# Kernel tuning notes

Hardware: AMD Instinct MI355X
Metric: run time of the kernel (lower is better)

The kernel has to match this reference:

```python
import jax, jax.numpy as jnp
import numpy as np

B, N, C, D = 64, 1024, 128, 64

def setup_inputs() -> dict:
    key = jax.random.key(0)
    ks = jax.random.split(key, 7)
    # kaiming_normal_ on weights (fan_in = C), default zero-ish biases kept as Linear default uniform; use small uniform
    std = float(np.sqrt(2.0 / C))
    bb = float(1.0 / np.sqrt(C))
    return {
        "x": jax.random.normal(ks[0], (B, N, C), jnp.float32),
        "Wq": jax.random.normal(ks[1], (C, D), jnp.float32) * std,
        "bq": jax.random.uniform(ks[2], (D,), jnp.float32, -bb, bb),
        "Wk": jax.random.normal(ks[3], (C, D), jnp.float32) * std,
        "bk": jax.random.uniform(ks[4], (D,), jnp.float32, -bb, bb),
        "Wv": jax.random.normal(ks[5], (C, D), jnp.float32) * std,
        "bv": jax.random.uniform(ks[6], (D,), jnp.float32, -bb, bb),
    }

def reference(x, Wq, bq, Wk, bk, Wv, bv):
    q = jax.nn.relu(jnp.einsum('bnc,cd->bnd', x, Wq) + bq)  # [B,N,D]
    k = jax.nn.relu(jnp.einsum('bnc,cd->bnd', x, Wk) + bk)
    v = jax.nn.relu(jnp.einsum('bnc,cd->bnd', x, Wv) + bv)
    scores = jnp.einsum('bnd,bmd->bnm', q, k) / jnp.sqrt(jnp.asarray(D, q.dtype))
    attn = jax.nn.softmax(scores, axis=-1)
    out = jnp.einsum('bnm,bmd->bnd', attn, v)
    return out + q
```

## Files before the change

kernel.cpp:

```cpp
#include <hip/hip_runtime.h>
#include <hip/hip_bf16.h>


#define Bsz 64
#define Nsz 1024
#define Csz 128
#define Dsz 64

typedef __attribute__((ext_vector_type(8))) short short8;
typedef __attribute__((ext_vector_type(4))) float f32x4;

__device__ __forceinline__ unsigned short f2bf(float f) {
    union { float f; unsigned u; } v; v.f = f;
    unsigned r = v.u + 0x7FFF + ((v.u >> 16) & 1);
    return (unsigned short)(r >> 16);
}
__device__ __forceinline__ float bf2f(unsigned short h) {
    union { unsigned u; float f; } v; v.u = ((unsigned)h) << 16;
    return v.f;
}
__device__ __forceinline__ unsigned pack_bf16rn(float lo, float hi) {
    unsigned ulo = __float_as_uint(lo) + 0x8000u;
    unsigned uhi = __float_as_uint(hi) + 0x8000u;
    return __builtin_amdgcn_perm(uhi, ulo, 0x07060302u);
}
__device__ __forceinline__ void gl_lds16(const void* gsrc, void* ldst) {
    __builtin_amdgcn_global_load_lds(
        (const __attribute__((address_space(1))) unsigned int*)gsrc,
        (__attribute__((address_space(3))) unsigned int*)ldst, 16, 0, 0);
}

#define SCq (0.125f * 1.44269504f)
#define INV_SC (1.0f / (0.125f * 1.44269504f))

__global__ __launch_bounds__(256) void wprep_kernel(
    const float* __restrict__ Wq, const float* __restrict__ Wk,
    const float* __restrict__ Wv, unsigned short* __restrict__ wfrag)
{
    int t = blockIdx.x * 256 + threadIdx.x;
    int lane = t & 63, ksi = (t >> 6) & 3, dt = t >> 8;
    int l16 = lane & 15, quad = lane >> 4;
    int d = dt * 16 + l16;
    int c0 = ksi * 32 + quad * 8;
    short8 h8, l8, k8, v8;
    #pragma unroll
    for (int j = 0; j < 8; j++) {
        float w = Wq[(c0 + j) * Dsz + d];
        unsigned short h = f2bf(w);
        h8[j] = (short)h;
        l8[j] = (short)f2bf(w - bf2f(h));
        k8[j] = (short)f2bf(Wk[(c0 + j) * Dsz + d]);
        v8[j] = (short)f2bf(Wv[(c0 + j) * Dsz + d]);
    }
    int idx = (dt * 4 + ksi) * 64 + lane;
    ((short8*)wfrag)[0 * 1024 + idx] = h8;
    ((short8*)wfrag)[1 * 1024 + idx] = l8;
    ((short8*)wfrag)[2 * 1024 + idx] = k8;
    ((short8*)wfrag)[3 * 1024 + idx] = v8;
}

__global__ __launch_bounds__(256) void qkv_kernel(
    const float* __restrict__ x, const unsigned short* __restrict__ wfrag,
    const float* __restrict__ bq, const float* __restrict__ bk,
    const float* __restrict__ bv,
    unsigned short* __restrict__ qs, unsigned short* __restrict__ ksc,
    unsigned short* __restrict__ vt)
{
    __shared__ short xh[8192];
    __shared__ short xl[8192];
    const int t    = threadIdx.x;
    const int lane = t & 63;
    const int l16  = lane & 15, quad = lane >> 4;
    const int dt   = t >> 6;
    const long rowbase = (long)blockIdx.x * 128;
    const int d = dt * 16 + l16;

    short8 wqh[4], wql[4], wkf[4], wvf[4];
    #pragma unroll
    for (int ksi = 0; ksi < 4; ksi++) {
        int idx = (dt * 4 + ksi) * 64 + lane;
        wqh[ksi] = ((const short8*)wfrag)[0 * 1024 + idx];
        wql[ksi] = ((const short8*)wfrag)[1 * 1024 + idx];
        wkf[ksi] = ((const short8*)wfrag)[2 * 1024 + idx];
        wvf[ksi] = ((const short8*)wfrag)[3 * 1024 + idx];
    }
    const float bqd = bq[d], bkd = bk[d], bvd = bv[d];
    const long b = rowbase >> 10;

    for (int chunk = 0; chunk < 2; chunk++) {
        const long rowc = rowbase + chunk * 64;
        if (chunk) __syncthreads();

        {
            const int row = t & 63;
            const float* xrow = x + (rowc + row) * Csz;
            #pragma unroll
            for (int p = 0; p < 4; p++) {
                int cb = (t >> 6) + p * 4;
                float4 a = *(const float4*)(xrow + cb * 8);
                float4 bb = *(const float4*)(xrow + cb * 8 + 4);
                float f[8] = {a.x, a.y, a.z, a.w, bb.x, bb.y, bb.z, bb.w};
                short8 hi, lo;
                #pragma unroll
                for (int i = 0; i < 8; i++) {
                    unsigned short h = f2bf(f[i]);
                    hi[i] = (short)h;
                    lo[i] = (short)f2bf(f[i] - bf2f(h));
                }
                int unit = ((row >> 4) * 4 + (cb >> 2)) * 64 + ((row & 15) | ((cb & 3) << 4));
                *(short8*)&xh[unit * 8] = hi;
                *(short8*)&xl[unit * 8] = lo;
            }
        }
        __syncthreads();

        f32x4 aq[4], ak[4], av[4];
        #pragma unroll
        for (int i = 0; i < 4; i++) {
            aq[i] = (f32x4){0.f, 0.f, 0.f, 0.f};
            ak[i] = (f32x4){0.f, 0.f, 0.f, 0.f};
            av[i] = (f32x4){0.f, 0.f, 0.f, 0.f};
        }
        #pragma unroll
        for (int ksi = 0; ksi < 4; ksi++) {
            #pragma unroll
            for (int rt = 0; rt < 4; rt++) {
                short8 ah = *(const short8*)&xh[((rt * 4 + ksi) * 64 + lane) * 8];
                short8 al = *(const short8*)&xl[((rt * 4 + ksi) * 64 + lane) * 8];
                aq[rt] = __builtin_amdgcn_mfma_f32_16x16x32_bf16(ah, wqh[ksi], aq[rt], 0, 0, 0);
                aq[rt] = __builtin_amdgcn_mfma_f32_16x16x32_bf16(al, wqh[ksi], aq[rt], 0, 0, 0);
                aq[rt] = __builtin_amdgcn_mfma_f32_16x16x32_bf16(ah, wql[ksi], aq[rt], 0, 0, 0);
                ak[rt] = __builtin_amdgcn_mfma_f32_16x16x32_bf16(ah, wkf[ksi], ak[rt], 0, 0, 0);
                av[rt] = __builtin_amdgcn_mfma_f32_16x16x32_bf16(ah, wvf[ksi], av[rt], 0, 0, 0);
            }
        }

        float vv[16];
        #pragma unroll
        for (int rt = 0; rt < 4; rt++) {
            #pragma unroll
            for (int r = 0; r < 4; r++) {
                long n = rowc + rt * 16 + quad * 4 + r;
                float q = fmaxf(aq[rt][r] + bqd, 0.f);
                float k = fmaxf(ak[rt][r] + bkd, 0.f);
                float v = fmaxf(av[rt][r] + bvd, 0.f);
                qs[n * Dsz + d]  = f2bf(q * SCq);
                ksc[n * Dsz + d] = f2bf(k);
                vv[r * 4 + rt] = v;
            }
        }
        unsigned short* vp = vt + b * (Dsz * Nsz) + (long)d * Nsz + (rowc & 1023) + quad * 16;
        uint4 p0 = make_uint4(pack_bf16rn(vv[0], vv[1]),  pack_bf16rn(vv[2], vv[3]),
                              pack_bf16rn(vv[4], vv[5]),  pack_bf16rn(vv[6], vv[7]));
        uint4 p1 = make_uint4(pack_bf16rn(vv[8], vv[9]),  pack_bf16rn(vv[10], vv[11]),
                              pack_bf16rn(vv[12], vv[13]), pack_bf16rn(vv[14], vv[15]));
        *(uint4*)vp = p0;
        *(uint4*)(vp + 8) = p1;
    }
}

__global__ __launch_bounds__(256) void attn_kernel(
    const unsigned short* __restrict__ qs,
    const unsigned short* __restrict__ ksc,
    const unsigned short* __restrict__ vt,
    float* __restrict__ out)
{
    __shared__ short tiles[4][4096];
    __shared__ short Pl[4][32][72];

    const int t    = threadIdx.x;
    const int wave = t >> 6;
    const int lane = t & 63;
    const int l16  = lane & 15;
    const int quad = lane >> 4;
    const int b    = blockIdx.x & 63;
    const int qh   = blockIdx.x >> 6;
    const int qbase = qh * 128 + wave * 32;

    const unsigned short* kb_ = ksc + (long)b * (Nsz * Dsz);
    const unsigned short* vb_ = vt  + (long)b * (Dsz * Nsz);

    auto issue = [&](int kt, int bufi) {
        const unsigned short* kg = kb_ + (long)kt * 64 * Dsz;
        const unsigned short* vg = vb_ + kt * 64;
        #pragma unroll
        for (int i = 0; i < 2; i++) {
            int seg  = wave * 2 + i;
            int slot = seg * 64 + lane;
            int rw = slot >> 3, pc = slot & 7, c = pc ^ (rw & 7);
            gl_lds16(kg + rw * Dsz + c * 8, &tiles[bufi * 2][seg * 512]);
            gl_lds16(vg + (long)rw * Nsz + c * 8, &tiles[bufi * 2 + 1][seg * 512]);
        }
    };

    short8 aq[2][2];
    #pragma unroll
    for (int s = 0; s < 2; s++) {
        const unsigned short* qp = qs + ((long)b * Nsz + qbase + s * 16 + l16) * Dsz + quad * 8;
        aq[s][0] = *(const short8*)(qp);
        aq[s][1] = *(const short8*)(qp + 32);
    }

    f32x4 O[2][4];
    float lsum[2][4];
    #pragma unroll
    for (int s = 0; s < 2; s++)
        #pragma unroll
        for (int i = 0; i < 4; i++) { O[s][i] = (f32x4){0.f,0.f,0.f,0.f}; lsum[s][i] = 0.f; }

    issue(0, 0);

    for (int kt = 0; kt < 16; kt++) {
        const int cur = kt & 1;
        __syncthreads();
        if (kt < 15) issue(kt + 1, 1 - cur);

        const short* Kt  = &tiles[cur * 2][0];
        const short* Vtl = &tiles[cur * 2 + 1][0];

        short8 kf[4][2];
        #pragma unroll
        for (int kb = 0; kb < 4; kb++) {
            int row = kb * 16 + l16;
            kf[kb][0] = *(const short8*)(Kt + (row * 8 + ( quad      ^ (l16 & 7))) * 8);
            kf[kb][1] = *(const short8*)(Kt + (row * 8 + ((4 + quad) ^ (l16 & 7))) * 8);
        }
        short8 bvf[2][4];
        #pragma unroll
        for (int ck = 0; ck < 2; ck++) {
            #pragma unroll
            for (int cb = 0; cb < 4; cb++) {
                int dim = cb * 16 + l16;
                bvf[ck][cb] = *(const short8*)(Vtl + (dim * 8 + ((ck * 4 + quad) ^ (l16 & 7))) * 8);
            }
        }

        #pragma unroll
        for (int s = 0; s < 2; s++) {
            f32x4 sc[4];
            #pragma unroll
            for (int kb = 0; kb < 4; kb++) {
                f32x4 z = (f32x4){0.f, 0.f, 0.f, 0.f};
                z = __builtin_amdgcn_mfma_f32_16x16x32_bf16(aq[s][0], kf[kb][0], z, 0, 0, 0);
                z = __builtin_amdgcn_mfma_f32_16x16x32_bf16(aq[s][1], kf[kb][1], z, 0, 0, 0);
                sc[kb] = z;
            }
            #pragma unroll
            for (int r = 0; r < 4; r++) {
                float p0 = __builtin_amdgcn_exp2f(sc[0][r]);
                float p1 = __builtin_amdgcn_exp2f(sc[1][r]);
                float p2 = __builtin_amdgcn_exp2f(sc[2][r]);
                float p3 = __builtin_amdgcn_exp2f(sc[3][r]);
                lsum[s][r] += (p0 + p1) + (p2 + p3);
                *(uint2*)&Pl[wave][s * 16 + quad * 4 + r][l16 * 4] =
                    make_uint2(pack_bf16rn(p0, p1), pack_bf16rn(p2, p3));
            }
        }

        #pragma unroll
        for (int ck = 0; ck < 2; ck++) {
            #pragma unroll
            for (int s = 0; s < 2; s++) {
                short8 ap = *(const short8*)&Pl[wave][s * 16 + l16][ck * 32 + quad * 8];
                #pragma unroll
                for (int cb = 0; cb < 4; cb++) {
                    O[s][cb] = __builtin_amdgcn_mfma_f32_16x16x32_bf16(ap, bvf[ck][cb], O[s][cb], 0, 0, 0);
                }
            }
        }
    }

    #pragma unroll
    for (int s = 0; s < 2; s++)
        #pragma unroll
        for (int r = 0; r < 4; r++)
            #pragma unroll
            for (int off = 1; off < 16; off <<= 1)
                lsum[s][r] += __shfl_xor(lsum[s][r], off);

    #pragma unroll
    for (int s = 0; s < 2; s++) {
        #pragma unroll
        for (int r = 0; r < 4; r++) {
            float rl = 1.0f / lsum[s][r];
            long nrow = (long)b * Nsz + qbase + s * 16 + quad * 4 + r;
            #pragma unroll
            for (int cb = 0; cb < 4; cb++) {
                int d = cb * 16 + l16;
                float qv = bf2f(qs[nrow * Dsz + d]) * INV_SC;
                out[nrow * Dsz + d] = O[s][cb][r] * rl + qv;
            }
        }
    }
}

extern "C" void kernel_launch(void* const* d_in, const int* in_sizes, int n_in,
                              void* d_out, int out_size, void* d_ws, size_t ws_size,
                              hipStream_t stream) {
    const float* x  = (const float*)d_in[0];
    const float* Wq = (const float*)d_in[1];
    const float* bq = (const float*)d_in[2];
    const float* Wk = (const float*)d_in[3];
    const float* bk = (const float*)d_in[4];
    const float* Wv = (const float*)d_in[5];
    const float* bv = (const float*)d_in[6];
    float* out = (float*)d_out;

    char* ws = (char*)d_ws;
    unsigned short* qsc   = (unsigned short*)ws;
    unsigned short* kscp  = (unsigned short*)(ws + 0x1000000);
    unsigned short* vtc   = (unsigned short*)(ws + 0x2000000);
    unsigned short* wfrag = (unsigned short*)(ws + 0x3000000);

    wprep_kernel<<<dim3(4), dim3(256), 0, stream>>>(Wq, Wk, Wv, wfrag);
    qkv_kernel<<<dim3(512), dim3(256), 0, stream>>>(
        x, wfrag, bq, bk, bv, qsc, kscp, vtc);
    attn_kernel<<<dim3(512), dim3(256), 0, stream>>>(
        qsc, kscp, vtc, out);
}
```

Measured before the change: 126.9 us.

## Store K and V pre-swizzled in MFMA fragment order, drop LDS staging in attention

The QKV kernel now writes K and V straight into the per-lane MFMA fragment layout, so the attention kernel can load B operands directly from global memory as short8 per lane. This removes the LDS tile buffers, the async global-to-LDS copies and the per-tile barriers. K fragments for the next tile are prefetched into registers. The QKV kernel also processes 64 rows per block across twice as many blocks instead of looping over two chunks. The trade-off is that every wave reads K/V from global or L2 on its own rather than sharing a block-wide LDS copy, which raises cache traffic and register pressure.

```diff
diff --git a/kernel.cpp b/kernel.cpp
--- a/kernel.cpp
+++ b/kernel.cpp
@@ -23,11 +23,6 @@
     unsigned ulo = __float_as_uint(lo) + 0x8000u;
     unsigned uhi = __float_as_uint(hi) + 0x8000u;
     return __builtin_amdgcn_perm(uhi, ulo, 0x07060302u);
-}
-__device__ __forceinline__ void gl_lds16(const void* gsrc, void* ldst) {
-    __builtin_amdgcn_global_load_lds(
-        (const __attribute__((address_space(1))) unsigned int*)gsrc,
-        (__attribute__((address_space(3))) unsigned int*)ldst, 16, 0, 0);
 }
 
 #define SCq (0.125f * 1.44269504f)
@@ -63,8 +58,8 @@
     const float* __restrict__ x, const unsigned short* __restrict__ wfrag,
     const float* __restrict__ bq, const float* __restrict__ bk,
     const float* __restrict__ bv,
-    unsigned short* __restrict__ qs, unsigned short* __restrict__ ksc,
-    unsigned short* __restrict__ vt)
+    unsigned short* __restrict__ qs, unsigned short* __restrict__ ks2,
+    unsigned short* __restrict__ vt2)
 {
     __shared__ short xh[8192];
     __shared__ short xl[8192];
@@ -72,7 +67,7 @@
     const int lane = t & 63;
     const int l16  = lane & 15, quad = lane >> 4;
     const int dt   = t >> 6;
-    const long rowbase = (long)blockIdx.x * 128;
+    const long rowbase = (long)blockIdx.x * 64;
     const int d = dt * 16 + l16;
 
     short8 wqh[4], wql[4], wkf[4], wvf[4];
@@ -84,88 +79,90 @@
         wkf[ksi] = ((const short8*)wfrag)[2 * 1024 + idx];
         wvf[ksi] = ((const short8*)wfrag)[3 * 1024 + idx];
     }
+
+    {
+        const int row = t & 63;
+        const float* xrow = x + (rowbase + row) * Csz;
+        #pragma unroll
+        for (int p = 0; p < 4; p++) {
+            int cb = (t >> 6) + p * 4;
+            float4 a = *(const float4*)(xrow + cb * 8);
+            float4 bb = *(const float4*)(xrow + cb * 8 + 4);
+            float f[8] = {a.x, a.y, a.z, a.w, bb.x, bb.y, bb.z, bb.w};
+            short8 hi, lo;
+            #pragma unroll
+            for (int i = 0; i < 8; i++) {
+                unsigned short h = f2bf(f[i]);
+                hi[i] = (short)h;
+                lo[i] = (short)f2bf(f[i] - bf2f(h));
+            }
+            int unit = ((row >> 4) * 4 + (cb >> 2)) * 64 + ((row & 15) | ((cb & 3) << 4));
+            *(short8*)&xh[unit * 8] = hi;
+            *(short8*)&xl[unit * 8] = lo;
+        }
+    }
+    __syncthreads();
+
+    f32x4 aq[4], ak[4], av[4];
+    #pragma unroll
+    for (int i = 0; i < 4; i++) {
+        aq[i] = (f32x4){0.f, 0.f, 0.f, 0.f};
+        ak[i] = (f32x4){0.f, 0.f, 0.f, 0.f};
+        av[i] = (f32x4){0.f, 0.f, 0.f, 0.f};
+    }
+    #pragma unroll
+    for (int ksi = 0; ksi < 4; ksi++) {
+        #pragma unroll
+        for (int rt = 0; rt < 4; rt++) {
+            short8 ah = *(const short8*)&xh[((rt * 4 + ksi) * 64 + lane) * 8];
+            short8 al = *(const short8*)&xl[((rt * 4 + ksi) * 64 + lane) * 8];
+            aq[rt] = __builtin_amdgcn_mfma_f32_16x16x32_bf16(ah, wqh[ksi], aq[rt], 0, 0, 0);
+            aq[rt] = __builtin_amdgcn_mfma_f32_16x16x32_bf16(al, wqh[ksi], aq[rt], 0, 0, 0);
+            aq[rt] = __builtin_amdgcn_mfma_f32_16x16x32_bf16(ah, wql[ksi], aq[rt], 0, 0, 0);
+            ak[rt] = __builtin_amdgcn_mfma_f32_16x16x32_bf16(ah, wkf[ksi], ak[rt], 0, 0, 0);
+            av[rt] = __builtin_amdgcn_mfma_f32_16x16x32_bf16(ah, wvf[ksi], av[rt], 0, 0, 0);
+        }
+    }
+
     const float bqd = bq[d], bkd = bk[d], bvd = bv[d];
-    const long b = rowbase >> 10;
-
-    for (int chunk = 0; chunk < 2; chunk++) {
-        const long rowc = rowbase + chunk * 64;
-        if (chunk) __syncthreads();
-
-        {
-            const int row = t & 63;
-            const float* xrow = x + (rowc + row) * Csz;
-            #pragma unroll
-            for (int p = 0; p < 4; p++) {
-                int cb = (t >> 6) + p * 4;
-                float4 a = *(const float4*)(xrow + cb * 8);
-                float4 bb = *(const float4*)(xrow + cb * 8 + 4);
-                float f[8] = {a.x, a.y, a.z, a.w, bb.x, bb.y, bb.z, bb.w};
-                short8 hi, lo;
-                #pragma unroll
-                for (int i = 0; i < 8; i++) {
-                    unsigned short h = f2bf(f[i]);
-                    hi[i] = (short)h;
-                    lo[i] = (short)f2bf(f[i] - bf2f(h));
-                }
-                int unit = ((row >> 4) * 4 + (cb >> 2)) * 64 + ((row & 15) | ((cb & 3) << 4));
-                *(short8*)&xh[unit * 8] = hi;
-                *(short8*)&xl[unit * 8] = lo;
-            }
-        }
-        __syncthreads();
-
-        f32x4 aq[4], ak[4], av[4];
-        #pragma unroll
-        for (int i = 0; i < 4; i++) {
-            aq[i] = (f32x4){0.f, 0.f, 0.f, 0.f};
-            ak[i] = (f32x4){0.f, 0.f, 0.f, 0.f};
-            av[i] = (f32x4){0.f, 0.f, 0.f, 0.f};
-        }
-        #pragma unroll
-        for (int ksi = 0; ksi < 4; ksi++) {
-            #pragma unroll
-            for (int rt = 0; rt < 4; rt++) {
-                short8 ah = *(const short8*)&xh[((rt * 4 + ksi) * 64 + lane) * 8];
-                short8 al = *(const short8*)&xl[((rt * 4 + ksi) * 64 + lane) * 8];
-                aq[rt] = __builtin_amdgcn_mfma_f32_16x16x32_bf16(ah, wqh[ksi], aq[rt], 0, 0, 0);
-                aq[rt] = __builtin_amdgcn_mfma_f32_16x16x32_bf16(al, wqh[ksi], aq[rt], 0, 0, 0);
-                aq[rt] = __builtin_amdgcn_mfma_f32_16x16x32_bf16(ah, wql[ksi], aq[rt], 0, 0, 0);
-                ak[rt] = __builtin_amdgcn_mfma_f32_16x16x32_bf16(ah, wkf[ksi], ak[rt], 0, 0, 0);
-                av[rt] = __builtin_amdgcn_mfma_f32_16x16x32_bf16(ah, wvf[ksi], av[rt], 0, 0, 0);
-            }
-        }
-
-        float vv[16];
-        #pragma unroll
-        for (int rt = 0; rt < 4; rt++) {
-            #pragma unroll
-            for (int r = 0; r < 4; r++) {
-                long n = rowc + rt * 16 + quad * 4 + r;
-                float q = fmaxf(aq[rt][r] + bqd, 0.f);
-                float k = fmaxf(ak[rt][r] + bkd, 0.f);
-                float v = fmaxf(av[rt][r] + bvd, 0.f);
-                qs[n * Dsz + d]  = f2bf(q * SCq);
-                ksc[n * Dsz + d] = f2bf(k);
-                vv[r * 4 + rt] = v;
-            }
-        }
-        unsigned short* vp = vt + b * (Dsz * Nsz) + (long)d * Nsz + (rowc & 1023) + quad * 16;
-        uint4 p0 = make_uint4(pack_bf16rn(vv[0], vv[1]),  pack_bf16rn(vv[2], vv[3]),
-                              pack_bf16rn(vv[4], vv[5]),  pack_bf16rn(vv[6], vv[7]));
-        uint4 p1 = make_uint4(pack_bf16rn(vv[8], vv[9]),  pack_bf16rn(vv[10], vv[11]),
-                              pack_bf16rn(vv[12], vv[13]), pack_bf16rn(vv[14], vv[15]));
-        *(uint4*)vp = p0;
-        *(uint4*)(vp + 8) = p1;
-    }
+    const long b  = rowbase >> 10;
+    const int  kt = (int)((rowbase >> 6) & 15);
+
+    const int half  = dt >> 1;
+    const int quadk = ((dt & 1) << 1) | (l16 >> 3);
+    const int jk    = l16 & 7;
+    unsigned short* kbase = ks2 + ((((long)(b * 16 + kt) * 4) * 2 + half) * 64) * 8;
+
+    float vv[4][4];
+    #pragma unroll
+    for (int rt = 0; rt < 4; rt++) {
+        #pragma unroll
+        for (int r = 0; r < 4; r++) {
+            long n = rowbase + rt * 16 + quad * 4 + r;
+            float q = fmaxf(aq[rt][r] + bqd, 0.f);
+            float k = fmaxf(ak[rt][r] + bkd, 0.f);
+            vv[r][rt] = fmaxf(av[rt][r] + bvd, 0.f);
+            qs[n * Dsz + d] = f2bf(q * SCq);
+            kbase[((long)rt * 2 * 64 + quadk * 16 + quad * 4 + r) * 8 + jk] = f2bf(k);
+        }
+    }
+    const int ck = quad >> 1;
+    const int quadp = (quad & 1) * 2;
+    long vidx = (((long)(b * 16 + kt) * 4 + dt) * 2 + ck) * 64 + quadp * 16 + l16;
+    uint4 o0 = make_uint4(pack_bf16rn(vv[0][0], vv[0][1]), pack_bf16rn(vv[0][2], vv[0][3]),
+                          pack_bf16rn(vv[1][0], vv[1][1]), pack_bf16rn(vv[1][2], vv[1][3]));
+    uint4 o1 = make_uint4(pack_bf16rn(vv[2][0], vv[2][1]), pack_bf16rn(vv[2][2], vv[2][3]),
+                          pack_bf16rn(vv[3][0], vv[3][1]), pack_bf16rn(vv[3][2], vv[3][3]));
+    ((uint4*)vt2)[vidx]      = o0;
+    ((uint4*)vt2)[vidx + 16] = o1;
 }
 
 __global__ __launch_bounds__(256) void attn_kernel(
     const unsigned short* __restrict__ qs,
-    const unsigned short* __restrict__ ksc,
-    const unsigned short* __restrict__ vt,
+    const unsigned short* __restrict__ ks2,
+    const unsigned short* __restrict__ vt2,
     float* __restrict__ out)
 {
-    __shared__ short tiles[4][4096];
     __shared__ short Pl[4][32][72];
 
     const int t    = threadIdx.x;
@@ -177,21 +174,8 @@
     const int qh   = blockIdx.x >> 6;
     const int qbase = qh * 128 + wave * 32;
 
-    const unsigned short* kb_ = ksc + (long)b * (Nsz * Dsz);
-    const unsigned short* vb_ = vt  + (long)b * (Dsz * Nsz);
-
-    auto issue = [&](int kt, int bufi) {
-        const unsigned short* kg = kb_ + (long)kt * 64 * Dsz;
-        const unsigned short* vg = vb_ + kt * 64;
-        #pragma unroll
-        for (int i = 0; i < 2; i++) {
-            int seg  = wave * 2 + i;
-            int slot = seg * 64 + lane;
-            int rw = slot >> 3, pc = slot & 7, c = pc ^ (rw & 7);
-            gl_lds16(kg + rw * Dsz + c * 8, &tiles[bufi * 2][seg * 512]);
-            gl_lds16(vg + (long)rw * Nsz + c * 8, &tiles[bufi * 2 + 1][seg * 512]);
-        }
-    };
+    const short8* ks8 = (const short8*)ks2 + (long)b * (16 * 4 * 2 * 64);
+    const short8* vt8 = (const short8*)vt2 + (long)b * (16 * 4 * 2 * 64);
 
     short8 aq[2][2];
     #pragma unroll
@@ -208,49 +192,51 @@
         #pragma unroll
         for (int i = 0; i < 4; i++) { O[s][i] = (f32x4){0.f,0.f,0.f,0.f}; lsum[s][i] = 0.f; }
 
-    issue(0, 0);
+    short8 kf[4][2];
+    #pragma unroll
+    for (int kb = 0; kb < 4; kb++) {
+        kf[kb][0] = ks8[(kb * 2 + 0) * 64 + lane];
+        kf[kb][1] = ks8[(kb * 2 + 1) * 64 + lane];
+    }
 
     for (int kt = 0; kt < 16; kt++) {
-        const int cur = kt & 1;
-        __syncthreads();
-        if (kt < 15) issue(kt + 1, 1 - cur);
-
-        const short* Kt  = &tiles[cur * 2][0];
-        const short* Vtl = &tiles[cur * 2 + 1][0];
-
-        short8 kf[4][2];
-        #pragma unroll
-        for (int kb = 0; kb < 4; kb++) {
-            int row = kb * 16 + l16;
-            kf[kb][0] = *(const short8*)(Kt + (row * 8 + ( quad      ^ (l16 & 7))) * 8);
-            kf[kb][1] = *(const short8*)(Kt + (row * 8 + ((4 + quad) ^ (l16 & 7))) * 8);
-        }
         short8 bvf[2][4];
         #pragma unroll
-        for (int ck = 0; ck < 2; ck++) {
-            #pragma unroll
-            for (int cb = 0; cb < 4; cb++) {
-                int dim = cb * 16 + l16;
-                bvf[ck][cb] = *(const short8*)(Vtl + (dim * 8 + ((ck * 4 + quad) ^ (l16 & 7))) * 8);
-            }
-        }
-
+        for (int cb = 0; cb < 4; cb++) {
+            bvf[0][cb] = vt8[((long)kt * 8 + cb * 2 + 0) * 64 + lane];
+            bvf[1][cb] = vt8[((long)kt * 8 + cb * 2 + 1) * 64 + lane];
+        }
+
+        f32x4 sc[2][4];
         #pragma unroll
         for (int s = 0; s < 2; s++) {
-            f32x4 sc[4];
             #pragma unroll
             for (int kb = 0; kb < 4; kb++) {
                 f32x4 z = (f32x4){0.f, 0.f, 0.f, 0.f};
                 z = __builtin_amdgcn_mfma_f32_16x16x32_bf16(aq[s][0], kf[kb][0], z, 0, 0, 0);
                 z = __builtin_amdgcn_mfma_f32_16x16x32_bf16(aq[s][1], kf[kb][1], z, 0, 0, 0);
-                sc[kb] = z;
-            }
+                sc[s][kb] = z;
+            }
+        }
+
+        short8 kf2[4][2];
+        {
+            int ktn = (kt + 1) & 15;
+            #pragma unroll
+            for (int kb = 0; kb < 4; kb++) {
+                kf2[kb][0] = ks8[((long)ktn * 8 + kb * 2 + 0) * 64 + lane];
+                kf2[kb][1] = ks8[((long)ktn * 8 + kb * 2 + 1) * 64 + lane];
+            }
+        }
+
+        #pragma unroll
+        for (int s = 0; s < 2; s++) {
             #pragma unroll
             for (int r = 0; r < 4; r++) {
-                float p0 = __builtin_amdgcn_exp2f(sc[0][r]);
-                float p1 = __builtin_amdgcn_exp2f(sc[1][r]);
-                float p2 = __builtin_amdgcn_exp2f(sc[2][r]);
-                float p3 = __builtin_amdgcn_exp2f(sc[3][r]);
+                float p0 = __builtin_amdgcn_exp2f(sc[s][0][r]);
+                float p1 = __builtin_amdgcn_exp2f(sc[s][1][r]);
+                float p2 = __builtin_amdgcn_exp2f(sc[s][2][r]);
+                float p3 = __builtin_amdgcn_exp2f(sc[s][3][r]);
                 lsum[s][r] += (p0 + p1) + (p2 + p3);
                 *(uint2*)&Pl[wave][s * 16 + quad * 4 + r][l16 * 4] =
                     make_uint2(pack_bf16rn(p0, p1), pack_bf16rn(p2, p3));
@@ -268,6 +254,9 @@
                 }
             }
         }
+
+        #pragma unroll
+        for (int kb = 0; kb < 4; kb++) { kf[kb][0] = kf2[kb][0]; kf[kb][1] = kf2[kb][1]; }
     }
 
     #pragma unroll
@@ -308,13 +297,13 @@
 
     char* ws = (char*)d_ws;
     unsigned short* qsc   = (unsigned short*)ws;
-    unsigned short* kscp  = (unsigned short*)(ws + 0x1000000);
-    unsigned short* vtc   = (unsigned short*)(ws + 0x2000000);
+    unsigned short* ks2   = (unsigned short*)(ws + 0x1000000);
+    unsigned short* vt2   = (unsigned short*)(ws + 0x2000000);
     unsigned short* wfrag = (unsigned short*)(ws + 0x3000000);
 
     wprep_kernel<<<dim3(4), dim3(256), 0, stream>>>(Wq, Wk, Wv, wfrag);
-    qkv_kernel<<<dim3(512), dim3(256), 0, stream>>>(
-        x, wfrag, bq, bk, bv, qsc, kscp, vtc);
+    qkv_kernel<<<dim3(1024), dim3(256), 0, stream>>>(
+        x, wfrag, bq, bk, bv, qsc, ks2, vt2);
     attn_kernel<<<dim3(512), dim3(256), 0, stream>>>(
-        qsc, kscp, vtc, out);
-}
+        qsc, ks2, vt2, out);
+}
```

Measured after the change: 121.8 us. 1.04x faster.
